# Kernel optimization log

Measured on AMD Instinct MI355X. Metric: run time of the kernel, lower is better.

The kernel has to match this reference:

```python
import jax, jax.numpy as jnp
import numpy as np

SEQ, D_IN, D_OUT = 8192, 768, 768

def setup_inputs() -> dict:
    key = jax.random.key(0)
    k1, k2, k3, k4 = jax.random.split(key, 4)
    scale = 1.0 / np.sqrt(D_IN)
    return {
        "x": jax.random.normal(k1, (SEQ, D_IN), dtype=jnp.float32),
        "w_q": jax.random.normal(k2, (D_OUT, D_IN), dtype=jnp.float32) * scale,
        "w_k": jax.random.normal(k3, (D_OUT, D_IN), dtype=jnp.float32) * scale,
        "w_v": jax.random.normal(k4, (D_OUT, D_IN), dtype=jnp.float32) * scale,
    }

def reference(x, w_q, w_k, w_v):
    # torch Linear: y = x @ W.T (no bias since qkv_bias=False)
    q = x @ w_q.T  # [S, D]
    k = x @ w_k.T  # [S, D]
    v = x @ w_v.T  # [S, D]
    scores = (q @ k.T) / jnp.sqrt(jnp.asarray(k.shape[-1], x.dtype))  # [S, S]
    attn = jax.nn.softmax(scores, axis=-1)
    return attn @ v  # [S, D]
```

## Files before the change

kernel.cpp:

```cpp
#include <hip/hip_runtime.h>

#define SEQ 8192
#define DIM 768

typedef __attribute__((ext_vector_type(8))) short s16x8;
typedef __attribute__((ext_vector_type(4))) float f32x4;

__device__ __forceinline__ unsigned short f2bf(float f) {
  union { float f; unsigned u; } v; v.f = f;
  unsigned r = v.u + 0x7FFFu + ((v.u >> 16) & 1u);
  return (unsigned short)(r >> 16);
}

__device__ __forceinline__ float bf2f(unsigned short s) {
  union { unsigned u; float f; } v; v.u = ((unsigned)s) << 16;
  return v.f;
}

__device__ __forceinline__ void gll16(const void* gsrc, void* ldst) {
  __builtin_amdgcn_global_load_lds(
      (__attribute__((address_space(1))) unsigned int*)gsrc,
      (__attribute__((address_space(3))) unsigned int*)ldst, 16, 0, 0);
}

#define XN4 (SEQ * DIM / 4)
#define WN4 (DIM * DIM / 4)

__global__ void cast_all_kernel(const float* __restrict__ x, const float* __restrict__ wq,
                                const float* __restrict__ wk, const float* __restrict__ wv,
                                unsigned short* __restrict__ dx, unsigned short* __restrict__ dq,
                                unsigned short* __restrict__ dk, unsigned short* __restrict__ dv) {
  int i = blockIdx.x * blockDim.x + threadIdx.x;
  const float* s;
  unsigned short* d;
  int off;
  if (i < XN4) {
    s = x; d = dx; off = i;
  } else {
    int j = i - XN4;
    int wi = j / WN4;
    off = j - wi * WN4;
    s = (wi == 0) ? wq : ((wi == 1) ? wk : wv);
    d = (wi == 0) ? dq : ((wi == 1) ? dk : dv);
  }
  float4 v = ((const float4*)s)[off];
  ushort4 r; r.x = f2bf(v.x); r.y = f2bf(v.y); r.z = f2bf(v.z); r.w = f2bf(v.w);
  ((ushort4*)d)[off] = r;
}

__global__ __launch_bounds__(256, 2)
void proj_kernel(const unsigned short* __restrict__ X,
                 const unsigned short* __restrict__ Wq,
                 const unsigned short* __restrict__ Wk,
                 const unsigned short* __restrict__ Wv,
                 unsigned short* __restrict__ Qb,
                 unsigned short* __restrict__ Kb,
                 unsigned short* __restrict__ Vtb) {
  __shared__ __align__(16) char lds[65536];
  const int tid = threadIdx.x;
  const int lane = tid & 63, wv = tid >> 6;
  const int l15 = lane & 15, l4 = lane >> 4;
  const int mt = blockIdx.x, nt = blockIdx.y, z = blockIdx.z;
  const unsigned short* W = (z == 0) ? Wq : ((z == 1) ? Wk : Wv);

  f32x4 acc[4][4];
#pragma unroll
  for (int i = 0; i < 4; ++i)
#pragma unroll
    for (int j = 0; j < 4; ++j) acc[i][j] = f32x4{0.f, 0.f, 0.f, 0.f};

  auto stage = [&](int kk) {
    char* At = lds + (kk & 1) * 32768;
    char* Bt = At + 16384;
    const int d0 = kk * 64;
#pragma unroll
    for (int i = 0; i < 4; ++i) {
      int s = i * 256 + tid;
      int row = s >> 3, c = (s & 7) ^ (row & 7);
      gll16(X + (long)(mt * 128 + row) * DIM + d0 + c * 8, At + i * 4096 + (wv << 10));
      gll16(W + (long)(nt * 128 + row) * DIM + d0 + c * 8, Bt + i * 4096 + (wv << 10));
    }
  };

  stage(0);
#pragma unroll 1
  for (int kk = 0; kk < 12; ++kk) {
    __syncthreads();
    if (kk + 1 < 12) stage(kk + 1);
    const char* At = lds + (kk & 1) * 32768;
    const char* Bt = At + 16384;
#pragma unroll
    for (int ks = 0; ks < 2; ++ks) {
      const int c = ks * 4 + l4;
      s16x8 a[4], b[4];
#pragma unroll
      for (int mi = 0; mi < 4; ++mi) {
        int row = (wv & 1) * 64 + mi * 16 + l15;
        a[mi] = *(const s16x8*)(At + row * 128 + ((c ^ (row & 7)) << 4));
      }
#pragma unroll
      for (int ni = 0; ni < 4; ++ni) {
        int row = (wv >> 1) * 64 + ni * 16 + l15;
        b[ni] = *(const s16x8*)(Bt + row * 128 + ((c ^ (row & 7)) << 4));
      }
#pragma unroll
      for (int mi = 0; mi < 4; ++mi)
#pragma unroll
        for (int ni = 0; ni < 4; ++ni)
          acc[mi][ni] = __builtin_amdgcn_mfma_f32_16x16x32_bf16(a[mi], b[ni], acc[mi][ni], 0, 0, 0);
    }
  }

#pragma unroll
  for (int mi = 0; mi < 4; ++mi)
#pragma unroll
    for (int ni = 0; ni < 4; ++ni) {
      int row0 = mt * 128 + (wv & 1) * 64 + mi * 16 + l4 * 4;
      int col = nt * 128 + (wv >> 1) * 64 + ni * 16 + l15;
      if (z == 2) {
        ushort4 r;
        r.x = f2bf(acc[mi][ni][0]); r.y = f2bf(acc[mi][ni][1]);
        r.z = f2bf(acc[mi][ni][2]); r.w = f2bf(acc[mi][ni][3]);
        *(ushort4*)(Vtb + (long)col * SEQ + row0) = r;
      } else {
        unsigned short* dst = (z == 0) ? Qb : Kb;
#pragma unroll
        for (int g = 0; g < 4; ++g)
          dst[(long)(row0 + g) * DIM + col] = f2bf(acc[mi][ni][g]);
      }
    }
}

#define SCALE_LOG2E 0.05205878f

__global__ __launch_bounds__(512, 2)
void flash_kernel(const unsigned short* __restrict__ Q,
                  const unsigned short* __restrict__ K,
                  const unsigned short* __restrict__ V,
                  unsigned short* __restrict__ partp,
                  float* __restrict__ outf,
                  float* __restrict__ lout,
                  int kv_len, int norm_out) {
  __shared__ __align__(16) char lds[80 * 1024 + 32 * 1024 + 1024];
  char* arena = lds;
  char* Pl = lds + 81920;
  float* l_part = (float*)(lds + 81920 + 32768);

  const int tid = threadIdx.x;
  const int lane = tid & 63, wv = tid >> 6;
  const int l15 = lane & 15, l4 = lane >> 4;
  const int qtile = blockIdx.x, split = blockIdx.y;
  const long kv0 = (long)split * kv_len;
  const long qrow0 = (long)qtile * 64;
  const int R = wv & 1;
  const int C = wv >> 1;

  f32x4 acc_o[4][6];
  float acc_lp[8];
#pragma unroll
  for (int i = 0; i < 4; ++i)
#pragma unroll
    for (int j = 0; j < 6; ++j) acc_o[i][j] = f32x4{0.f, 0.f, 0.f, 0.f};
#pragma unroll
  for (int i = 0; i < 8; ++i) acc_lp[i] = 0.f;

  const int niter = kv_len >> 8;

#pragma unroll 1
  for (int it = 0; it < niter; ++it) {
    const long kb = kv0 + (long)it * 256;

    auto stageQK = [&](int r) {
      char* Qc = arena + (r & 1) * 40960;
      char* Kc = Qc + 8192;
      const int d0 = r * 64;
      {
        int s = tid;
        int row = s >> 3, c = (s & 7) ^ (row & 7);
        gll16(Q + (qrow0 + row) * DIM + d0 + c * 8, Qc + (wv << 10));
      }
#pragma unroll
      for (int i = 0; i < 4; ++i) {
        int s = i * 512 + tid;
        int row = s >> 3, c = (s & 7) ^ (row & 7);
        gll16(K + (kb + row) * DIM + d0 + c * 8, Kc + i * 8192 + (wv << 10));
      }
    };
    auto stagePV = [&](int r) {
      char* Vc = arena + (r & 1) * 32768;
      const int cc_ = r >> 2, kh_ = r & 3;
#pragma unroll
      for (int i = 0; i < 4; ++i) {
        int s = i * 512 + tid;
        int vr = s >> 3, c = (s & 7) ^ (vr & 7);
        gll16(V + (long)(cc_ * 256 + vr) * SEQ + kb + kh_ * 64 + c * 8, Vc + i * 8192 + (wv << 10));
      }
    };

    f32x4 acc_s[2][4];
#pragma unroll
    for (int a = 0; a < 2; ++a)
#pragma unroll
      for (int b = 0; b < 4; ++b) acc_s[a][b] = f32x4{0.f, 0.f, 0.f, 0.f};

    stageQK(0);
#pragma unroll 1
    for (int r = 0; r < 12; ++r) {
      __syncthreads();
      if (r + 1 < 12) stageQK(r + 1);
      const char* Qc = arena + (r & 1) * 40960;
      const char* Kc = Qc + 8192;
#pragma unroll
      for (int ks = 0; ks < 2; ++ks) {
        const int c = ks * 4 + l4;
        s16x8 af[2], bk[4];
#pragma unroll
        for (int rt = 0; rt < 2; ++rt) {
          int row = R * 32 + rt * 16 + l15;
          af[rt] = *(const s16x8*)(Qc + row * 128 + ((c ^ (row & 7)) << 4));
        }
#pragma unroll
        for (int ct = 0; ct < 4; ++ct) {
          int kr = C * 64 + ct * 16 + l15;
          bk[ct] = *(const s16x8*)(Kc + kr * 128 + ((c ^ (kr & 7)) << 4));
        }
#pragma unroll
        for (int rt = 0; rt < 2; ++rt)
#pragma unroll
          for (int ct = 0; ct < 4; ++ct)
            acc_s[rt][ct] = __builtin_amdgcn_mfma_f32_16x16x32_bf16(af[rt], bk[ct], acc_s[rt][ct], 0, 0, 0);
      }
    }

#pragma unroll
    for (int rt = 0; rt < 2; ++rt)
#pragma unroll
      for (int ct = 0; ct < 4; ++ct)
#pragma unroll
        for (int g = 0; g < 4; ++g) {
          float p = exp2f(acc_s[rt][ct][g] * SCALE_LOG2E);
          acc_lp[rt * 4 + g] += p;
          int row = R * 32 + rt * 16 + l4 * 4 + g;
          int col = C * 64 + ct * 16 + l15;
          int off = row * 512 + ((((col >> 3) ^ (row & 7))) << 4) + ((col & 7) << 1);
          *(unsigned short*)(Pl + off) = f2bf(p);
        }

    stagePV(0);
#pragma unroll
    for (int cc = 0; cc < 3; ++cc) {
#pragma unroll 1
      for (int kh = 0; kh < 4; ++kh) {
        const int r = cc * 4 + kh;
        __syncthreads();
        if (r + 1 < 12) stagePV(r + 1);
        const char* Vc = arena + (r & 1) * 32768;
#pragma unroll
        for (int ks = 0; ks < 2; ++ks) {
          s16x8 pa[4], vb[2];
          const int ck = kh * 8 + ks * 4 + l4;
#pragma unroll
          for (int rs = 0; rs < 4; ++rs) {
            int row = rs * 16 + l15;
            int pc = (ck & ~7) | ((ck & 7) ^ (row & 7));
            pa[rs] = *(const s16x8*)(Pl + row * 512 + (pc << 4));
          }
          const int cv = ks * 4 + l4;
#pragma unroll
          for (int t = 0; t < 2; ++t) {
            int vr = (wv + 8 * t) * 16 + l15;
            vb[t] = *(const s16x8*)(Vc + vr * 128 + ((cv ^ (vr & 7)) << 4));
          }
#pragma unroll
          for (int rs = 0; rs < 4; ++rs)
#pragma unroll
            for (int t = 0; t < 2; ++t)
              acc_o[rs][cc * 2 + t] =
                  __builtin_amdgcn_mfma_f32_16x16x32_bf16(pa[rs], vb[t], acc_o[rs][cc * 2 + t], 0, 0, 0);
        }
      }
    }
    __syncthreads();
  }

#pragma unroll
  for (int i = 0; i < 8; ++i) {
    float v = acc_lp[i];
    v += __shfl_xor(v, 1); v += __shfl_xor(v, 2);
    v += __shfl_xor(v, 4); v += __shfl_xor(v, 8);
    acc_lp[i] = v;
  }
  if (l15 == 0) {
#pragma unroll
    for (int rt = 0; rt < 2; ++rt)
#pragma unroll
      for (int g = 0; g < 4; ++g)
        l_part[C * 64 + R * 32 + rt * 16 + l4 * 4 + g] = acc_lp[rt * 4 + g];
  }
  __syncthreads();

  if (!norm_out) {
    if (tid < 64)
      lout[(long)split * SEQ + qrow0 + tid] =
          l_part[tid] + l_part[64 + tid] + l_part[128 + tid] + l_part[192 + tid];
#pragma unroll
    for (int rt = 0; rt < 4; ++rt) {
      int row = rt * 16 + l4 * 4;
#pragma unroll
      for (int j = 0; j < 6; ++j) {
        int cc = j >> 1, t = j & 1;
        int col = (cc * 16 + wv + 8 * t) * 16 + l15;
#pragma unroll
        for (int g = 0; g < 4; ++g)
          partp[(long)split * SEQ * DIM + (qrow0 + row + g) * DIM + col] = f2bf(acc_o[rt][j][g]);
      }
    }
  } else {
    float linv[4][4];
#pragma unroll
    for (int rt = 0; rt < 4; ++rt)
#pragma unroll
      for (int g = 0; g < 4; ++g) {
        int row = rt * 16 + l4 * 4 + g;
        linv[rt][g] = 1.0f / (l_part[row] + l_part[64 + row] + l_part[128 + row] + l_part[192 + row]);
      }
#pragma unroll
    for (int rt = 0; rt < 4; ++rt) {
      int row = rt * 16 + l4 * 4;
#pragma unroll
      for (int j = 0; j < 6; ++j) {
        int cc = j >> 1, t = j & 1;
        int col = (cc * 16 + wv + 8 * t) * 16 + l15;
#pragma unroll
        for (int g = 0; g < 4; ++g)
          outf[(qrow0 + row + g) * DIM + col] = acc_o[rt][j][g] * linv[rt][g];
      }
    }
  }
}

__global__ void combine_kernel(const unsigned short* __restrict__ part,
                               const float* __restrict__ lsum,
                               float* __restrict__ out, int n4) {
  int i = blockIdx.x * blockDim.x + threadIdx.x;
  if (i >= n4) return;
  int row = (i * 4) / DIM;
  ushort4 p0 = ((const ushort4*)part)[i];
  ushort4 p1 = ((const ushort4*)(part + (long)SEQ * DIM))[i];
  float inv = 1.0f / (lsum[row] + lsum[SEQ + row]);
  float4 o;
  o.x = (bf2f(p0.x) + bf2f(p1.x)) * inv;
  o.y = (bf2f(p0.y) + bf2f(p1.y)) * inv;
  o.z = (bf2f(p0.z) + bf2f(p1.z)) * inv;
  o.w = (bf2f(p0.w) + bf2f(p1.w)) * inv;
  ((float4*)out)[i] = o;
}

extern "C" void kernel_launch(void* const* d_in, const int* in_sizes, int n_in,
                              void* d_out, int out_size, void* d_ws, size_t ws_size,
                              hipStream_t stream) {
  const float* x = (const float*)d_in[0];
  const float* wq = (const float*)d_in[1];
  const float* wk = (const float*)d_in[2];
  const float* wv = (const float*)d_in[3];
  float* out = (float*)d_out;
  char* ws = (char*)d_ws;

  const size_t o_xbf = 0;
  const size_t o_wq = o_xbf + (size_t)SEQ * DIM * 2;
  const size_t o_wk = o_wq + (size_t)DIM * DIM * 2;
  const size_t o_wv = o_wk + (size_t)DIM * DIM * 2;
  const size_t o_q = o_wv + (size_t)DIM * DIM * 2;
  const size_t o_k = o_q + (size_t)SEQ * DIM * 2;
  const size_t o_vt = o_k + (size_t)SEQ * DIM * 2;
  const size_t o_part = o_vt + (size_t)SEQ * DIM * 2;
  const size_t o_l = o_part + (size_t)2 * SEQ * DIM * 2;
  const size_t total_g2 = o_l + (size_t)2 * SEQ * 4;

  unsigned short* Xbf = (unsigned short*)(ws + o_xbf);
  unsigned short* Wqb = (unsigned short*)(ws + o_wq);
  unsigned short* Wkb = (unsigned short*)(ws + o_wk);
  unsigned short* Wvb = (unsigned short*)(ws + o_wv);
  unsigned short* Qb = (unsigned short*)(ws + o_q);
  unsigned short* Kb = (unsigned short*)(ws + o_k);
  unsigned short* Vtb = (unsigned short*)(ws + o_vt);
  unsigned short* part = (unsigned short*)(ws + o_part);
  float* lbuf = (float*)(ws + o_l);

  const int G = (ws_size >= total_g2) ? 2 : 1;

  cast_all_kernel<<<7872, 256, 0, stream>>>(x, wq, wk, wv, Xbf, Wqb, Wkb, Wvb);
  proj_kernel<<<dim3(64, 6, 3), 256, 0, stream>>>(Xbf, Wqb, Wkb, Wvb, Qb, Kb, Vtb);
  if (G == 2) {
    flash_kernel<<<dim3(128, 2), 512, 0, stream>>>(Qb, Kb, Vtb, part, nullptr, lbuf, SEQ / 2, 0);
    combine_kernel<<<6144, 256, 0, stream>>>(part, lbuf, out, SEQ * DIM / 4);
  } else {
    flash_kernel<<<dim3(128, 1), 512, 0, stream>>>(Qb, Kb, Vtb, nullptr, out, nullptr, SEQ, 1);
  }
}
```

Before: 332.0 us.

## Triple-buffer QK/PV staging with vmcnt barriers across phases and iterations

Replaces double-buffered LDS staging, where every step waited on a full __syncthreads, with a three-slot ring. Loads are issued two steps ahead, and partial s_waitcnt vmcnt plus s_barrier let later loads stay in flight. The first QK stages of the next KV block are prefetched during the tail of the PV loop, and the first PV stages during the tail of the QK loop, so no pipeline drain happens at phase boundaries. MFMA sections are also wrapped in s_setprio. The cost is more LDS (about 153 KB), which may lower occupancy below the two blocks per CU targeted by launch bounds, plus fully unrolled loops that raise code size and register pressure.

```diff
diff --git a/kernel.cpp b/kernel.cpp
--- a/kernel.cpp
+++ b/kernel.cpp
@@ -21,6 +21,13 @@
   __builtin_amdgcn_global_load_lds(
       (__attribute__((address_space(1))) unsigned int*)gsrc,
       (__attribute__((address_space(3))) unsigned int*)ldst, 16, 0, 0);
+}
+
+template <int N>
+__device__ __forceinline__ void vm_bar() {
+  asm volatile("s_waitcnt vmcnt(%0)" ::"n"(N) : "memory");
+  __builtin_amdgcn_s_barrier();
+  __builtin_amdgcn_sched_barrier(0);
 }
 
 #define XN4 (SEQ * DIM / 4)
@@ -141,10 +148,9 @@
                   float* __restrict__ outf,
                   float* __restrict__ lout,
                   int kv_len, int norm_out) {
-  __shared__ __align__(16) char lds[80 * 1024 + 32 * 1024 + 1024];
-  char* arena = lds;
-  char* Pl = lds + 81920;
-  float* l_part = (float*)(lds + 81920 + 32768);
+  __shared__ __align__(16) char lds[3 * 40960 + 32768 + 1024];
+  char* Pl = lds + 3 * 40960;
+  float* l_part = (float*)(lds + 3 * 40960 + 32768);
 
   const int tid = threadIdx.x;
   const int lane = tid & 63, wv = tid >> 6;
@@ -166,36 +172,40 @@
 
   const int niter = kv_len >> 8;
 
+  auto stageQK = [&](int slot, int d0, long kb) {
+    char* Qc = lds + slot * 40960;
+    char* Kc = Qc + 8192;
+    {
+      int s = tid;
+      int row = s >> 3, c = (s & 7) ^ (row & 7);
+      gll16(Q + (qrow0 + row) * DIM + d0 + c * 8, Qc + (wv << 10));
+    }
+#pragma unroll
+    for (int i = 0; i < 4; ++i) {
+      int s = i * 512 + tid;
+      int row = s >> 3, c = (s & 7) ^ (row & 7);
+      gll16(K + (kb + row) * DIM + d0 + c * 8, Kc + i * 8192 + (wv << 10));
+    }
+  };
+  auto stagePV = [&](int slot, int r, long kb) {
+    char* Vc = lds + slot * 40960;
+    const int cc_ = r >> 2, kh_ = r & 3;
+#pragma unroll
+    for (int i = 0; i < 4; ++i) {
+      int s = i * 512 + tid;
+      int vr = s >> 3, c = (s & 7) ^ (vr & 7);
+      gll16(V + (long)(cc_ * 256 + vr) * SEQ + kb + kh_ * 64 + c * 8, Vc + i * 8192 + (wv << 10));
+    }
+  };
+
+  stageQK(0, 0, kv0);
+  stageQK(1, 64, kv0);
+  vm_bar<5>();
+
 #pragma unroll 1
   for (int it = 0; it < niter; ++it) {
     const long kb = kv0 + (long)it * 256;
-
-    auto stageQK = [&](int r) {
-      char* Qc = arena + (r & 1) * 40960;
-      char* Kc = Qc + 8192;
-      const int d0 = r * 64;
-      {
-        int s = tid;
-        int row = s >> 3, c = (s & 7) ^ (row & 7);
-        gll16(Q + (qrow0 + row) * DIM + d0 + c * 8, Qc + (wv << 10));
-      }
-#pragma unroll
-      for (int i = 0; i < 4; ++i) {
-        int s = i * 512 + tid;
-        int row = s >> 3, c = (s & 7) ^ (row & 7);
-        gll16(K + (kb + row) * DIM + d0 + c * 8, Kc + i * 8192 + (wv << 10));
-      }
-    };
-    auto stagePV = [&](int r) {
-      char* Vc = arena + (r & 1) * 32768;
-      const int cc_ = r >> 2, kh_ = r & 3;
-#pragma unroll
-      for (int i = 0; i < 4; ++i) {
-        int s = i * 512 + tid;
-        int vr = s >> 3, c = (s & 7) ^ (vr & 7);
-        gll16(V + (long)(cc_ * 256 + vr) * SEQ + kb + kh_ * 64 + c * 8, Vc + i * 8192 + (wv << 10));
-      }
-    };
+    const long kbn = kb + 256;
 
     f32x4 acc_s[2][4];
 #pragma unroll
@@ -203,12 +213,8 @@
 #pragma unroll
       for (int b = 0; b < 4; ++b) acc_s[a][b] = f32x4{0.f, 0.f, 0.f, 0.f};
 
-    stageQK(0);
-#pragma unroll 1
-    for (int r = 0; r < 12; ++r) {
-      __syncthreads();
-      if (r + 1 < 12) stageQK(r + 1);
-      const char* Qc = arena + (r & 1) * 40960;
+    auto qk_body = [&](int slot) {
+      const char* Qc = lds + slot * 40960;
       const char* Kc = Qc + 8192;
 #pragma unroll
       for (int ks = 0; ks < 2; ++ks) {
@@ -224,13 +230,55 @@
           int kr = C * 64 + ct * 16 + l15;
           bk[ct] = *(const s16x8*)(Kc + kr * 128 + ((c ^ (kr & 7)) << 4));
         }
+        __builtin_amdgcn_s_setprio(1);
 #pragma unroll
         for (int rt = 0; rt < 2; ++rt)
 #pragma unroll
           for (int ct = 0; ct < 4; ++ct)
             acc_s[rt][ct] = __builtin_amdgcn_mfma_f32_16x16x32_bf16(af[rt], bk[ct], acc_s[rt][ct], 0, 0, 0);
-      }
-    }
+        __builtin_amdgcn_s_setprio(0);
+      }
+    };
+    auto pv_body = [&](int slot, int cc, int kh) {
+      const char* Vc = lds + slot * 40960;
+#pragma unroll
+      for (int ks = 0; ks < 2; ++ks) {
+        s16x8 pa[4], vb[2];
+        const int ck = kh * 8 + ks * 4 + l4;
+#pragma unroll
+        for (int rs = 0; rs < 4; ++rs) {
+          int row = rs * 16 + l15;
+          int pc = (ck & ~7) | ((ck & 7) ^ (row & 7));
+          pa[rs] = *(const s16x8*)(Pl + row * 512 + (pc << 4));
+        }
+        const int cv = ks * 4 + l4;
+#pragma unroll
+        for (int t = 0; t < 2; ++t) {
+          int vr = (wv + 8 * t) * 16 + l15;
+          vb[t] = *(const s16x8*)(Vc + vr * 128 + ((cv ^ (vr & 7)) << 4));
+        }
+        __builtin_amdgcn_s_setprio(1);
+#pragma unroll
+        for (int rs = 0; rs < 4; ++rs)
+#pragma unroll
+          for (int t = 0; t < 2; ++t)
+            acc_o[rs][cc * 2 + t] =
+                __builtin_amdgcn_mfma_f32_16x16x32_bf16(pa[rs], vb[t], acc_o[rs][cc * 2 + t], 0, 0, 0);
+        __builtin_amdgcn_s_setprio(0);
+      }
+    };
+
+#pragma unroll
+    for (int r = 0; r < 10; ++r) {
+      stageQK((r + 2) % 3, (r + 2) * 64, kb);
+      qk_body(r % 3);
+      vm_bar<5>();
+    }
+    stagePV(0, 0, kb);
+    qk_body(1);
+    vm_bar<4>();
+    stagePV(1, 1, kb);
+    qk_body(2);
 
 #pragma unroll
     for (int rt = 0; rt < 2; ++rt)
@@ -245,42 +293,38 @@
           int off = row * 512 + ((((col >> 3) ^ (row & 7))) << 4) + ((col & 7) << 1);
           *(unsigned short*)(Pl + off) = f2bf(p);
         }
-
-    stagePV(0);
+    asm volatile("s_waitcnt lgkmcnt(0)" ::: "memory");
+    vm_bar<4>();
+
 #pragma unroll
     for (int cc = 0; cc < 3; ++cc) {
-#pragma unroll 1
+#pragma unroll
       for (int kh = 0; kh < 4; ++kh) {
         const int r = cc * 4 + kh;
-        __syncthreads();
-        if (r + 1 < 12) stagePV(r + 1);
-        const char* Vc = arena + (r & 1) * 32768;
-#pragma unroll
-        for (int ks = 0; ks < 2; ++ks) {
-          s16x8 pa[4], vb[2];
-          const int ck = kh * 8 + ks * 4 + l4;
-#pragma unroll
-          for (int rs = 0; rs < 4; ++rs) {
-            int row = rs * 16 + l15;
-            int pc = (ck & ~7) | ((ck & 7) ^ (row & 7));
-            pa[rs] = *(const s16x8*)(Pl + row * 512 + (pc << 4));
+        if (r < 10) {
+          stagePV((r + 2) % 3, r + 2, kb);
+          pv_body(r % 3, cc, kh);
+          vm_bar<4>();
+        } else if (r == 10) {
+          if (it + 1 < niter) {
+            stageQK(0, 0, kbn);
+            pv_body(1, cc, kh);
+            vm_bar<5>();
+          } else {
+            pv_body(1, cc, kh);
+            vm_bar<0>();
           }
-          const int cv = ks * 4 + l4;
-#pragma unroll
-          for (int t = 0; t < 2; ++t) {
-            int vr = (wv + 8 * t) * 16 + l15;
-            vb[t] = *(const s16x8*)(Vc + vr * 128 + ((cv ^ (vr & 7)) << 4));
+        } else {
+          if (it + 1 < niter) {
+            stageQK(1, 64, kbn);
+            pv_body(2, cc, kh);
+            vm_bar<5>();
+          } else {
+            pv_body(2, cc, kh);
           }
-#pragma unroll
-          for (int rs = 0; rs < 4; ++rs)
-#pragma unroll
-            for (int t = 0; t < 2; ++t)
-              acc_o[rs][cc * 2 + t] =
-                  __builtin_amdgcn_mfma_f32_16x16x32_bf16(pa[rs], vb[t], acc_o[rs][cc * 2 + t], 0, 0, 0);
-        }
-      }
-    }
-    __syncthreads();
+        }
+      }
+    }
   }
 
 #pragma unroll
```

Result: slower. 434.1 us (+30.7%).

## Load Q, K, V MFMA operands directly from global memory instead of LDS staging

Applied to the files above, without the earlier changes.

Removes the double-buffered LDS staging of Q/K and V tiles, including the global_load_lds copies and per-step barriers. Each wave now reads its MFMA fragments straight from global memory through L1/L2, and LDS shrinks to the P buffer. This is meant to cut barrier and LDS traffic and raise occupancy, but it gives up cross-wave reuse: Q and K fragments are re-read by several waves, and V reads become strided 16-byte gathers without the latency hiding that prefetching provided.

```diff
diff --git a/kernel.cpp b/kernel.cpp
--- a/kernel.cpp
+++ b/kernel.cpp
@@ -141,10 +141,9 @@
                   float* __restrict__ outf,
                   float* __restrict__ lout,
                   int kv_len, int norm_out) {
-  __shared__ __align__(16) char lds[80 * 1024 + 32 * 1024 + 1024];
-  char* arena = lds;
-  char* Pl = lds + 81920;
-  float* l_part = (float*)(lds + 81920 + 32768);
+  __shared__ __align__(16) char lds[32768 + 1024];
+  char* Pl = lds;
+  float* l_part = (float*)(lds + 32768);
 
   const int tid = threadIdx.x;
   const int lane = tid & 63, wv = tid >> 6;
@@ -166,64 +165,39 @@
 
   const int niter = kv_len >> 8;
 
+  const unsigned short* Qrow[2];
+#pragma unroll
+  for (int rt = 0; rt < 2; ++rt)
+    Qrow[rt] = Q + (qrow0 + R * 32 + rt * 16 + l15) * (long)DIM;
+  const unsigned short* Vrow[2];
+#pragma unroll
+  for (int t = 0; t < 2; ++t)
+    Vrow[t] = V + (long)((wv + 8 * t) * 16 + l15) * SEQ;
+
 #pragma unroll 1
   for (int it = 0; it < niter; ++it) {
     const long kb = kv0 + (long)it * 256;
 
-    auto stageQK = [&](int r) {
-      char* Qc = arena + (r & 1) * 40960;
-      char* Kc = Qc + 8192;
-      const int d0 = r * 64;
-      {
-        int s = tid;
-        int row = s >> 3, c = (s & 7) ^ (row & 7);
-        gll16(Q + (qrow0 + row) * DIM + d0 + c * 8, Qc + (wv << 10));
-      }
-#pragma unroll
-      for (int i = 0; i < 4; ++i) {
-        int s = i * 512 + tid;
-        int row = s >> 3, c = (s & 7) ^ (row & 7);
-        gll16(K + (kb + row) * DIM + d0 + c * 8, Kc + i * 8192 + (wv << 10));
-      }
-    };
-    auto stagePV = [&](int r) {
-      char* Vc = arena + (r & 1) * 32768;
-      const int cc_ = r >> 2, kh_ = r & 3;
-#pragma unroll
-      for (int i = 0; i < 4; ++i) {
-        int s = i * 512 + tid;
-        int vr = s >> 3, c = (s & 7) ^ (vr & 7);
-        gll16(V + (long)(cc_ * 256 + vr) * SEQ + kb + kh_ * 64 + c * 8, Vc + i * 8192 + (wv << 10));
-      }
-    };
-
     f32x4 acc_s[2][4];
 #pragma unroll
     for (int a = 0; a < 2; ++a)
 #pragma unroll
       for (int b = 0; b < 4; ++b) acc_s[a][b] = f32x4{0.f, 0.f, 0.f, 0.f};
 
-    stageQK(0);
-#pragma unroll 1
+    const unsigned short* Kbase = K + (kb + C * 64 + l15) * (long)DIM;
+
+#pragma unroll 2
     for (int r = 0; r < 12; ++r) {
-      __syncthreads();
-      if (r + 1 < 12) stageQK(r + 1);
-      const char* Qc = arena + (r & 1) * 40960;
-      const char* Kc = Qc + 8192;
 #pragma unroll
       for (int ks = 0; ks < 2; ++ks) {
-        const int c = ks * 4 + l4;
+        const int dc = r * 64 + (ks * 4 + l4) * 8;
         s16x8 af[2], bk[4];
 #pragma unroll
-        for (int rt = 0; rt < 2; ++rt) {
-          int row = R * 32 + rt * 16 + l15;
-          af[rt] = *(const s16x8*)(Qc + row * 128 + ((c ^ (row & 7)) << 4));
-        }
-#pragma unroll
-        for (int ct = 0; ct < 4; ++ct) {
-          int kr = C * 64 + ct * 16 + l15;
-          bk[ct] = *(const s16x8*)(Kc + kr * 128 + ((c ^ (kr & 7)) << 4));
-        }
+        for (int rt = 0; rt < 2; ++rt)
+          af[rt] = *(const s16x8*)(Qrow[rt] + dc);
+#pragma unroll
+        for (int ct = 0; ct < 4; ++ct)
+          bk[ct] = *(const s16x8*)(Kbase + (long)ct * 16 * DIM + dc);
 #pragma unroll
         for (int rt = 0; rt < 2; ++rt)
 #pragma unroll
@@ -245,16 +219,12 @@
           int off = row * 512 + ((((col >> 3) ^ (row & 7))) << 4) + ((col & 7) << 1);
           *(unsigned short*)(Pl + off) = f2bf(p);
         }
-
-    stagePV(0);
+    __syncthreads();
+
 #pragma unroll
     for (int cc = 0; cc < 3; ++cc) {
-#pragma unroll 1
+#pragma unroll 2
       for (int kh = 0; kh < 4; ++kh) {
-        const int r = cc * 4 + kh;
-        __syncthreads();
-        if (r + 1 < 12) stagePV(r + 1);
-        const char* Vc = arena + (r & 1) * 32768;
 #pragma unroll
         for (int ks = 0; ks < 2; ++ks) {
           s16x8 pa[4], vb[2];
@@ -265,12 +235,10 @@
             int pc = (ck & ~7) | ((ck & 7) ^ (row & 7));
             pa[rs] = *(const s16x8*)(Pl + row * 512 + (pc << 4));
           }
-          const int cv = ks * 4 + l4;
-#pragma unroll
-          for (int t = 0; t < 2; ++t) {
-            int vr = (wv + 8 * t) * 16 + l15;
-            vb[t] = *(const s16x8*)(Vc + vr * 128 + ((cv ^ (vr & 7)) << 4));
-          }
+          const long kcol = kb + kh * 64 + (ks * 4 + l4) * 8;
+#pragma unroll
+          for (int t = 0; t < 2; ++t)
+            vb[t] = *(const s16x8*)(Vrow[t] + (long)cc * 256 * SEQ + kcol);
 #pragma unroll
           for (int rs = 0; rs < 4; ++rs)
 #pragma unroll
```

After: 763.3 us. 130% more time.

## Switch PV stage to 32x32x16 MFMA with larger V tiles and overlapped prefetch

Applied to the files above, without the earlier changes.

Rewrites the P·V phase of the flash kernel to use 32x32x16 bf16 MFMA instructions with f32x16 accumulators instead of 16x16x32. V is staged as 32-key-column slabs covering all 768 output columns (48KB double buffers), which cuts the PV loop to 8 barriers from 12. The first V prefetch is issued during the last QK round so it overlaps with compute. The epilogue row/column mapping is changed to match the 32x32 accumulator layout. LDS grows to about 129KB, which may limit occupancy with launch bounds (512,2).

```diff
diff --git a/kernel.cpp b/kernel.cpp
--- a/kernel.cpp
+++ b/kernel.cpp
@@ -5,6 +5,7 @@
 
 typedef __attribute__((ext_vector_type(8))) short s16x8;
 typedef __attribute__((ext_vector_type(4))) float f32x4;
+typedef __attribute__((ext_vector_type(16))) float f32x16;
 
 __device__ __forceinline__ unsigned short f2bf(float f) {
   union { float f; unsigned u; } v; v.f = f;
@@ -141,26 +142,28 @@
                   float* __restrict__ outf,
                   float* __restrict__ lout,
                   int kv_len, int norm_out) {
-  __shared__ __align__(16) char lds[80 * 1024 + 32 * 1024 + 1024];
-  char* arena = lds;
-  char* Pl = lds + 81920;
-  float* l_part = (float*)(lds + 81920 + 32768);
+  __shared__ __align__(16) char lds[98304 + 32768 + 1024];
+  char* Pl = lds + 98304;
+  float* l_part = (float*)(lds + 131072);
 
   const int tid = threadIdx.x;
   const int lane = tid & 63, wv = tid >> 6;
   const int l15 = lane & 15, l4 = lane >> 4;
+  const int l31 = lane & 31, h = lane >> 5;
   const int qtile = blockIdx.x, split = blockIdx.y;
   const long kv0 = (long)split * kv_len;
   const long qrow0 = (long)qtile * 64;
   const int R = wv & 1;
   const int C = wv >> 1;
 
-  f32x4 acc_o[4][6];
+  f32x16 acc_o[2][3];
   float acc_lp[8];
 #pragma unroll
-  for (int i = 0; i < 4; ++i)
-#pragma unroll
-    for (int j = 0; j < 6; ++j) acc_o[i][j] = f32x4{0.f, 0.f, 0.f, 0.f};
+  for (int i = 0; i < 2; ++i)
+#pragma unroll
+    for (int j = 0; j < 3; ++j)
+#pragma unroll
+      for (int e = 0; e < 16; ++e) acc_o[i][j][e] = 0.f;
 #pragma unroll
   for (int i = 0; i < 8; ++i) acc_lp[i] = 0.f;
 
@@ -171,7 +174,7 @@
     const long kb = kv0 + (long)it * 256;
 
     auto stageQK = [&](int r) {
-      char* Qc = arena + (r & 1) * 40960;
+      char* Qc = lds + ((r & 1) ^ 1) * 40960;
       char* Kc = Qc + 8192;
       const int d0 = r * 64;
       {
@@ -186,14 +189,17 @@
         gll16(K + (kb + row) * DIM + d0 + c * 8, Kc + i * 8192 + (wv << 10));
       }
     };
-    auto stagePV = [&](int r) {
-      char* Vc = arena + (r & 1) * 32768;
-      const int cc_ = r >> 2, kh_ = r & 3;
-#pragma unroll
-      for (int i = 0; i < 4; ++i) {
-        int s = i * 512 + tid;
-        int vr = s >> 3, c = (s & 7) ^ (vr & 7);
-        gll16(V + (long)(cc_ * 256 + vr) * SEQ + kb + kh_ * 64 + c * 8, Vc + i * 8192 + (wv << 10));
+    auto stagePV = [&](int v) {
+      char* Vc = lds + ((v & 1) ^ 1) * 49152;
+      const long kcol = kb + v * 32;
+#pragma unroll
+      for (int i = 0; i < 6; ++i) {
+        int linear = i * 512 + tid;
+        int rp = linear >> 3, p3 = linear & 7;
+        int orig = p3 ^ (rp & 7);
+        int vr = rp * 2 + (orig >> 2);
+        int k8 = orig & 3;
+        gll16(V + (long)vr * SEQ + kcol + k8 * 8, Vc + i * 8192 + (wv << 10));
       }
     };
 
@@ -208,7 +214,8 @@
     for (int r = 0; r < 12; ++r) {
       __syncthreads();
       if (r + 1 < 12) stageQK(r + 1);
-      const char* Qc = arena + (r & 1) * 40960;
+      else stagePV(0);
+      const char* Qc = lds + ((r & 1) ^ 1) * 40960;
       const char* Kc = Qc + 8192;
 #pragma unroll
       for (int ks = 0; ks < 2; ++ks) {
@@ -246,38 +253,33 @@
           *(unsigned short*)(Pl + off) = f2bf(p);
         }
 
-    stagePV(0);
-#pragma unroll
-    for (int cc = 0; cc < 3; ++cc) {
 #pragma unroll 1
-      for (int kh = 0; kh < 4; ++kh) {
-        const int r = cc * 4 + kh;
-        __syncthreads();
-        if (r + 1 < 12) stagePV(r + 1);
-        const char* Vc = arena + (r & 1) * 32768;
-#pragma unroll
-        for (int ks = 0; ks < 2; ++ks) {
-          s16x8 pa[4], vb[2];
-          const int ck = kh * 8 + ks * 4 + l4;
-#pragma unroll
-          for (int rs = 0; rs < 4; ++rs) {
-            int row = rs * 16 + l15;
-            int pc = (ck & ~7) | ((ck & 7) ^ (row & 7));
-            pa[rs] = *(const s16x8*)(Pl + row * 512 + (pc << 4));
-          }
-          const int cv = ks * 4 + l4;
-#pragma unroll
-          for (int t = 0; t < 2; ++t) {
-            int vr = (wv + 8 * t) * 16 + l15;
-            vb[t] = *(const s16x8*)(Vc + vr * 128 + ((cv ^ (vr & 7)) << 4));
-          }
-#pragma unroll
-          for (int rs = 0; rs < 4; ++rs)
-#pragma unroll
-            for (int t = 0; t < 2; ++t)
-              acc_o[rs][cc * 2 + t] =
-                  __builtin_amdgcn_mfma_f32_16x16x32_bf16(pa[rs], vb[t], acc_o[rs][cc * 2 + t], 0, 0, 0);
-        }
+    for (int v = 0; v < 8; ++v) {
+      __syncthreads();
+      if (v + 1 < 8) stagePV(v + 1);
+      const char* Vc = lds + ((v & 1) ^ 1) * 49152;
+#pragma unroll
+      for (int s = 0; s < 2; ++s) {
+        const int kg = v * 4 + s * 2 + h;
+        s16x8 pa[2], vb[3];
+#pragma unroll
+        for (int rs = 0; rs < 2; ++rs) {
+          int row = rs * 32 + l31;
+          int pc = (kg & ~7) | ((kg & 7) ^ (row & 7));
+          pa[rs] = *(const s16x8*)(Pl + row * 512 + (pc << 4));
+        }
+#pragma unroll
+        for (int ct = 0; ct < 3; ++ct) {
+          int vr = wv * 32 + ct * 256 + l31;
+          int rp = vr >> 1;
+          int p3 = (((vr & 1) << 2) | (s * 2 + h)) ^ (rp & 7);
+          vb[ct] = *(const s16x8*)(Vc + rp * 128 + (p3 << 4));
+        }
+#pragma unroll
+        for (int rs = 0; rs < 2; ++rs)
+#pragma unroll
+          for (int ct = 0; ct < 3; ++ct)
+            acc_o[rs][ct] = __builtin_amdgcn_mfma_f32_32x32x16_bf16(pa[rs], vb[ct], acc_o[rs][ct], 0, 0, 0);
       }
     }
     __syncthreads();
@@ -304,38 +306,29 @@
       lout[(long)split * SEQ + qrow0 + tid] =
           l_part[tid] + l_part[64 + tid] + l_part[128 + tid] + l_part[192 + tid];
 #pragma unroll
-    for (int rt = 0; rt < 4; ++rt) {
-      int row = rt * 16 + l4 * 4;
-#pragma unroll
-      for (int j = 0; j < 6; ++j) {
-        int cc = j >> 1, t = j & 1;
-        int col = (cc * 16 + wv + 8 * t) * 16 + l15;
-#pragma unroll
-        for (int g = 0; g < 4; ++g)
-          partp[(long)split * SEQ * DIM + (qrow0 + row + g) * DIM + col] = f2bf(acc_o[rt][j][g]);
-      }
-    }
+    for (int rs = 0; rs < 2; ++rs)
+#pragma unroll
+      for (int reg = 0; reg < 16; ++reg) {
+        int row = rs * 32 + (reg & 3) + 8 * (reg >> 2) + 4 * h;
+#pragma unroll
+        for (int ct = 0; ct < 3; ++ct) {
+          int col = wv * 32 + ct * 256 + l31;
+          partp[(long)split * SEQ * DIM + (qrow0 + row) * DIM + col] = f2bf(acc_o[rs][ct][reg]);
+        }
+      }
   } else {
-    float linv[4][4];
-#pragma unroll
-    for (int rt = 0; rt < 4; ++rt)
-#pragma unroll
-      for (int g = 0; g < 4; ++g) {
-        int row = rt * 16 + l4 * 4 + g;
-        linv[rt][g] = 1.0f / (l_part[row] + l_part[64 + row] + l_part[128 + row] + l_part[192 + row]);
-      }
-#pragma unroll
-    for (int rt = 0; rt < 4; ++rt) {
-      int row = rt * 16 + l4 * 4;
-#pragma unroll
-      for (int j = 0; j < 6; ++j) {
-        int cc = j >> 1, t = j & 1;
-        int col = (cc * 16 + wv + 8 * t) * 16 + l15;
-#pragma unroll
-        for (int g = 0; g < 4; ++g)
-          outf[(qrow0 + row + g) * DIM + col] = acc_o[rt][j][g] * linv[rt][g];
-      }
-    }
+#pragma unroll
+    for (int rs = 0; rs < 2; ++rs)
+#pragma unroll
+      for (int reg = 0; reg < 16; ++reg) {
+        int row = rs * 32 + (reg & 3) + 8 * (reg >> 2) + 4 * h;
+        float inv = 1.0f / (l_part[row] + l_part[64 + row] + l_part[128 + row] + l_part[192 + row]);
+#pragma unroll
+        for (int ct = 0; ct < 3; ++ct) {
+          int col = wv * 32 + ct * 256 + l31;
+          outf[(qrow0 + row) * DIM + col] = acc_o[rs][ct][reg] * inv;
+        }
+      }
   }
 }
 
```

Result: slower. 366.0 us (+10.2%).
